# Kernel optimization log

Hardware: AMD Instinct MI355X
Metric: run time of the kernel (lower is better)

Reference implementation:

```python
import jax, jax.numpy as jnp
import numpy as np

N = 100000      # nodes
E = 1600000     # edges (avg degree 16)
D_IN, D_H, D_OUT = 128, 128, 64
NORM_SCALE = 1.0
EPS = 1e-6


def setup_inputs() -> dict:
    key = jax.random.key(0)
    ks = jax.random.split(key, 9)
    x = jax.random.normal(ks[0], (N, D_IN), dtype=jnp.float32)
    edge_index = jax.random.randint(ks[1], (2, E), 0, N, dtype=jnp.int32)
    edge_weight = jax.random.uniform(ks[2], (E,), dtype=jnp.float32)
    # GraphConv = Linear then spmm(adj, .); Glorot-ish init for weights
    W0 = jax.random.normal(ks[3], (D_IN, D_H), dtype=jnp.float32) / np.float32(np.sqrt(D_IN))
    b0 = jnp.zeros((D_H,), jnp.float32)
    W1 = jax.random.normal(ks[4], (D_H, D_H), dtype=jnp.float32) / np.float32(np.sqrt(D_H))
    b1 = jnp.zeros((D_H,), jnp.float32)
    Wout = jax.random.normal(ks[5], (D_H, D_OUT), dtype=jnp.float32) / np.float32(np.sqrt(D_H))
    bout = jnp.zeros((D_OUT,), jnp.float32)
    return {"x": x, "edge_index": edge_index, "edge_weight": edge_weight,
            "W0": W0, "b0": b0, "W1": W1, "b1": b1, "Wout": Wout, "bout": bout}


def _pair_norm(h):
    # PairNorm mode 'PN': center columns, divide by sqrt(mean squared row norm)
    h = h - jnp.mean(h, axis=0, keepdims=True)
    rownorm_mean = jnp.sqrt(EPS + jnp.mean(jnp.sum(h * h, axis=1)))
    return NORM_SCALE * h / rownorm_mean


def reference(x, edge_index, edge_weight, W0, b0, W1, b1, Wout, bout):
    src = edge_index[0]
    dst = edge_index[1]

    def graph_conv(h, W, b):
        h = h @ W + b                              # [N, d_out]
        msg = edge_weight[:, None] * h[src]        # [E, d_out] gather
        return jax.ops.segment_sum(msg, dst, num_segments=N)  # spmm(adj, h)

    x_old = jnp.zeros((), jnp.float32)
    for (W, b) in ((W0, b0), (W1, b1)):
        # dropout p=0 -> identity (omitted)
        h = graph_conv(x, W, b)
        h = jax.nn.relu(_pair_norm(h))
        x = h + x_old        # residual=1 -> skip every layer
        x_old = x
    return graph_conv(x, Wout, bout)
```

## Files before the change

### kernel.cpp

```cpp
#include <hip/hip_runtime.h>

#define N_NODES 100000
#define N_EDGES 1600000
#define DH 128
#define DOUT 64
#define EPS 1e-6f
#define NBINS 8
#define BINW 12500
#define NREP 64

__device__ inline unsigned bfround(float f) {
    unsigned u = __float_as_uint(f);
    return (u + 0x7fffu + ((u >> 16) & 1u)) >> 16;
}
__device__ inline unsigned pack2(float a, float b) { return bfround(a) | (bfround(b) << 16); }
__device__ inline float blo(unsigned u) { return __uint_as_float(u << 16); }
__device__ inline float bhi(unsigned u) { return __uint_as_float(u & 0xffff0000u); }

template <int COLS, int PN, bool OUTBF>
__global__ __launch_bounds__(256) void gemm_kernel(const float* __restrict__ Xa,
                                                   const float* __restrict__ muA,
                                                   const float* __restrict__ invA,
                                                   const float* __restrict__ Xb,
                                                   const float* __restrict__ muB,
                                                   const float* __restrict__ invB,
                                                   const float* __restrict__ W,
                                                   const float* __restrict__ bias,
                                                   void* __restrict__ Yv, int nrows) {
    constexpr int K = 128;
    constexpr int BK = 64;
    constexpr int COLG = COLS / 8;
    constexpr int ROWG = 256 / COLG;
    constexpr int RPT = 64 / ROWG;

    __shared__ float wlds[BK * COLS];
    __shared__ float xlds[64][BK + 1];

    const int tid = threadIdx.x;
    const int row0 = blockIdx.x * 64;

    const float sA = (PN >= 1) ? invA[0] : 0.f;
    const float sB = (PN == 2) ? invB[0] : 0.f;

    const int colg = tid % COLG;
    const int rowg = tid / COLG;
    const int c0 = colg * 8;
    const int r0 = rowg * RPT;

    float acc[RPT][8];
#pragma unroll
    for (int i = 0; i < RPT; ++i)
#pragma unroll
        for (int j = 0; j < 8; ++j) acc[i][j] = 0.f;

    for (int kb = 0; kb < K; kb += BK) {
        constexpr int WVEC = BK * COLS / 4;
        for (int i = tid; i < WVEC; i += 256) {
            int kr = i / (COLS / 4);
            int c4 = i % (COLS / 4);
            reinterpret_cast<float4*>(wlds)[i] =
                reinterpret_cast<const float4*>(W)[(size_t)(kb + kr) * (COLS / 4) + c4];
        }
        for (int i = tid; i < 64 * (BK / 4); i += 256) {
            int r = i / (BK / 4);
            int c4 = i % (BK / 4);
            int col4 = kb / 4 + c4;
            float4 v = make_float4(0.f, 0.f, 0.f, 0.f);
            if (row0 + r < nrows) {
                v = reinterpret_cast<const float4*>(Xa + (size_t)(row0 + r) * K)[col4];
                if constexpr (PN >= 1) {
                    float4 m = reinterpret_cast<const float4*>(muA)[col4];
                    v.x = fmaxf((v.x - m.x) * sA, 0.f);
                    v.y = fmaxf((v.y - m.y) * sA, 0.f);
                    v.z = fmaxf((v.z - m.z) * sA, 0.f);
                    v.w = fmaxf((v.w - m.w) * sA, 0.f);
                }
                if constexpr (PN == 2) {
                    float4 v2 = reinterpret_cast<const float4*>(Xb + (size_t)(row0 + r) * K)[col4];
                    float4 m2 = reinterpret_cast<const float4*>(muB)[col4];
                    v.x += fmaxf((v2.x - m2.x) * sB, 0.f);
                    v.y += fmaxf((v2.y - m2.y) * sB, 0.f);
                    v.z += fmaxf((v2.z - m2.z) * sB, 0.f);
                    v.w += fmaxf((v2.w - m2.w) * sB, 0.f);
                }
            }
            xlds[r][c4 * 4 + 0] = v.x;
            xlds[r][c4 * 4 + 1] = v.y;
            xlds[r][c4 * 4 + 2] = v.z;
            xlds[r][c4 * 4 + 3] = v.w;
        }
        __syncthreads();

        for (int k = 0; k < BK; ++k) {
            float4 w0 = *reinterpret_cast<const float4*>(&wlds[k * COLS + c0]);
            float4 w1 = *reinterpret_cast<const float4*>(&wlds[k * COLS + c0 + 4]);
#pragma unroll
            for (int i = 0; i < RPT; ++i) {
                float xv = xlds[r0 + i][k];
                acc[i][0] += xv * w0.x;
                acc[i][1] += xv * w0.y;
                acc[i][2] += xv * w0.z;
                acc[i][3] += xv * w0.w;
                acc[i][4] += xv * w1.x;
                acc[i][5] += xv * w1.y;
                acc[i][6] += xv * w1.z;
                acc[i][7] += xv * w1.w;
            }
        }
        __syncthreads();
    }

    float bv[8];
#pragma unroll
    for (int j = 0; j < 8; ++j) bv[j] = bias[c0 + j];

#pragma unroll
    for (int i = 0; i < RPT; ++i) {
        int row = row0 + r0 + i;
        if (row < nrows) {
#pragma unroll
            for (int j = 0; j < 8; ++j) acc[i][j] += bv[j];
            if constexpr (OUTBF) {
                uint4 q;
                q.x = pack2(acc[i][0], acc[i][1]);
                q.y = pack2(acc[i][2], acc[i][3]);
                q.z = pack2(acc[i][4], acc[i][5]);
                q.w = pack2(acc[i][6], acc[i][7]);
                *reinterpret_cast<uint4*>((unsigned*)Yv + (size_t)row * (COLS / 2) + (c0 >> 1)) = q;
            } else {
                float4 o0 = make_float4(acc[i][0], acc[i][1], acc[i][2], acc[i][3]);
                float4 o1 = make_float4(acc[i][4], acc[i][5], acc[i][6], acc[i][7]);
                float4* yp = reinterpret_cast<float4*>((float*)Yv + (size_t)row * COLS + c0);
                yp[0] = o0;
                yp[1] = o1;
            }
        }
    }
}

__global__ __launch_bounds__(256) void hist_kernel(const int* __restrict__ dst,
                                                   int* __restrict__ counts) {
    int e = blockIdx.x * blockDim.x + threadIdx.x;
    const int stride = gridDim.x * blockDim.x;
    for (; e < N_EDGES; e += stride) atomicAdd(&counts[dst[e]], 1);
}

__global__ __launch_bounds__(1024) void scan_kernel(const int* __restrict__ counts,
                                                    int* __restrict__ rowptr) {
    __shared__ int wsum[16];
    const int tid = threadIdx.x;
    const int lane = tid & 63;
    const int w = tid >> 6;
    int offset = 0;
    if (tid == 0) rowptr[0] = 0;
    for (int base = 0; base < N_NODES; base += 4096) {
        int i = base + tid * 4;
        int4 v = make_int4(0, 0, 0, 0);
        if (i < N_NODES) v = *reinterpret_cast<const int4*>(counts + i);
        int p0 = v.x, p1 = p0 + v.y, p2 = p1 + v.z, p3 = p2 + v.w;
        int incl = p3;
#pragma unroll
        for (int d = 1; d < 64; d <<= 1) {
            int t = __shfl_up(incl, d, 64);
            if (lane >= d) incl += t;
        }
        if (lane == 63) wsum[w] = incl;
        __syncthreads();
        if (w == 0 && lane < 16) {
            int t = wsum[lane];
#pragma unroll
            for (int d = 1; d < 16; d <<= 1) {
                int u = __shfl_up(t, d, 64);
                if (lane >= d) t += u;
            }
            wsum[lane] = t;
        }
        __syncthreads();
        int woff = (w == 0) ? 0 : wsum[w - 1];
        int chunk_total = wsum[15];
        int tbase = offset + woff + incl - p3;
        if (i < N_NODES) {
            rowptr[i + 1] = tbase + p0;
            rowptr[i + 2] = tbase + p1;
            rowptr[i + 3] = tbase + p2;
            rowptr[i + 4] = tbase + p3;
        }
        offset += chunk_total;
        __syncthreads();
    }
}

__global__ __launch_bounds__(256) void bucket_kernel(const int* __restrict__ src,
                                                     const int* __restrict__ dst,
                                                     const float* __restrict__ ew,
                                                     const int* __restrict__ rowptr,
                                                     int* __restrict__ fill,
                                                     int2* __restrict__ em) {
    const int myBin = blockIdx.x & (NBINS - 1);
    const int lo = myBin * BINW;
    const int hi = lo + BINW;
    int e = (blockIdx.x >> 3) * 256 + threadIdx.x;
    const int stride = (gridDim.x >> 3) * 256;
    for (; e < N_EDGES; e += stride) {
        int d = dst[e];
        if (d >= lo && d < hi) {
            int pos = atomicAdd(&fill[d], 1);
            em[rowptr[d] + pos] = make_int2(src[e], __float_as_int(ew[e]));
        }
    }
}

__global__ __launch_bounds__(256) void agg128b_kernel(const unsigned* __restrict__ Hb,
                                                      const int* __restrict__ rowptr,
                                                      const int2* __restrict__ em,
                                                      float* __restrict__ B,
                                                      float* __restrict__ cs_part,
                                                      float* __restrict__ ss_part) {
    __shared__ int2 smeta[4][64];
    __shared__ float cs[4][128];
    __shared__ float ssw[4];
    const int wv = threadIdx.x >> 6;
    const int lane = threadIdx.x & 63;
    const int node = blockIdx.x * 4 + wv;
    const int beg = rowptr[node];
    const int end = rowptr[node + 1];
    const int2* sm = smeta[wv];
    float ax0 = 0.f, ay0 = 0.f, ax1 = 0.f, ay1 = 0.f;

    for (int c = beg; c < end; c += 64) {
        smeta[wv][lane] = (c + lane < end) ? em[c + lane] : make_int2(0, 0);
        const int cnt = min(64, end - c);
        const int rounds = (cnt + 7) >> 3;
        for (int g = 0; g < rounds; ++g) {
            int2 m0 = sm[g * 8 + 0];
            int2 m1 = sm[g * 8 + 1];
            int2 m2 = sm[g * 8 + 2];
            int2 m3 = sm[g * 8 + 3];
            int2 m4 = sm[g * 8 + 4];
            int2 m5 = sm[g * 8 + 5];
            int2 m6 = sm[g * 8 + 6];
            int2 m7 = sm[g * 8 + 7];
            unsigned u0 = Hb[(size_t)m0.x * 64 + lane];
            unsigned u1 = Hb[(size_t)m1.x * 64 + lane];
            unsigned u2 = Hb[(size_t)m2.x * 64 + lane];
            unsigned u3 = Hb[(size_t)m3.x * 64 + lane];
            unsigned u4 = Hb[(size_t)m4.x * 64 + lane];
            unsigned u5 = Hb[(size_t)m5.x * 64 + lane];
            unsigned u6 = Hb[(size_t)m6.x * 64 + lane];
            unsigned u7 = Hb[(size_t)m7.x * 64 + lane];
            float w0 = __int_as_float(m0.y), w1 = __int_as_float(m1.y);
            float w2 = __int_as_float(m2.y), w3 = __int_as_float(m3.y);
            float w4 = __int_as_float(m4.y), w5 = __int_as_float(m5.y);
            float w6 = __int_as_float(m6.y), w7 = __int_as_float(m7.y);
            ax0 += w0 * blo(u0); ay0 += w0 * bhi(u0);
            ax1 += w1 * blo(u1); ay1 += w1 * bhi(u1);
            ax0 += w2 * blo(u2); ay0 += w2 * bhi(u2);
            ax1 += w3 * blo(u3); ay1 += w3 * bhi(u3);
            ax0 += w4 * blo(u4); ay0 += w4 * bhi(u4);
            ax1 += w5 * blo(u5); ay1 += w5 * bhi(u5);
            ax0 += w6 * blo(u6); ay0 += w6 * bhi(u6);
            ax1 += w7 * blo(u7); ay1 += w7 * bhi(u7);
        }
    }
    float2 acc = make_float2(ax0 + ax1, ay0 + ay1);
    reinterpret_cast<float2*>(B + (size_t)node * DH)[lane] = acc;

    cs[wv][lane * 2] = acc.x;
    cs[wv][lane * 2 + 1] = acc.y;
    float sq = acc.x * acc.x + acc.y * acc.y;
#pragma unroll
    for (int off = 32; off; off >>= 1) sq += __shfl_down(sq, off, 64);
    if (lane == 0) ssw[wv] = sq;
    __syncthreads();
    const int rep = blockIdx.x & (NREP - 1);
    if (threadIdx.x < 128) {
        float s = cs[0][threadIdx.x] + cs[1][threadIdx.x] + cs[2][threadIdx.x] + cs[3][threadIdx.x];
        atomicAdd(&cs_part[rep * 128 + threadIdx.x], s);
    }
    if (threadIdx.x == 0) atomicAdd(&ss_part[rep], ssw[0] + ssw[1] + ssw[2] + ssw[3]);
}

__global__ __launch_bounds__(256) void agg64b_kernel(const unsigned* __restrict__ Hb,
                                                     const int* __restrict__ rowptr,
                                                     const int2* __restrict__ em,
                                                     float* __restrict__ out) {
    __shared__ int2 smeta[4][64];
    const int wv = threadIdx.x >> 6;
    const int lane = threadIdx.x & 63;
    const int half = lane >> 5;
    const int col = lane & 31;
    const int node = blockIdx.x * 4 + wv;
    const int beg = rowptr[node];
    const int end = rowptr[node + 1];
    const int2* sm = smeta[wv];
    float ax0 = 0.f, ay0 = 0.f, ax1 = 0.f, ay1 = 0.f;

    for (int c = beg; c < end; c += 64) {
        smeta[wv][lane] = (c + lane < end) ? em[c + lane] : make_int2(0, 0);
        const int cnt = min(64, end - c);
        const int rounds = (cnt + 15) >> 4;
        for (int g = 0; g < rounds; ++g) {
            const int b = g * 16 + half;
            int2 m0 = sm[b + 0];
            int2 m1 = sm[b + 2];
            int2 m2 = sm[b + 4];
            int2 m3 = sm[b + 6];
            int2 m4 = sm[b + 8];
            int2 m5 = sm[b + 10];
            int2 m6 = sm[b + 12];
            int2 m7 = sm[b + 14];
            unsigned u0 = Hb[(size_t)m0.x * 32 + col];
            unsigned u1 = Hb[(size_t)m1.x * 32 + col];
            unsigned u2 = Hb[(size_t)m2.x * 32 + col];
            unsigned u3 = Hb[(size_t)m3.x * 32 + col];
            unsigned u4 = Hb[(size_t)m4.x * 32 + col];
            unsigned u5 = Hb[(size_t)m5.x * 32 + col];
            unsigned u6 = Hb[(size_t)m6.x * 32 + col];
            unsigned u7 = Hb[(size_t)m7.x * 32 + col];
            float w0 = __int_as_float(m0.y), w1 = __int_as_float(m1.y);
            float w2 = __int_as_float(m2.y), w3 = __int_as_float(m3.y);
            float w4 = __int_as_float(m4.y), w5 = __int_as_float(m5.y);
            float w6 = __int_as_float(m6.y), w7 = __int_as_float(m7.y);
            ax0 += w0 * blo(u0); ay0 += w0 * bhi(u0);
            ax1 += w1 * blo(u1); ay1 += w1 * bhi(u1);
            ax0 += w2 * blo(u2); ay0 += w2 * bhi(u2);
            ax1 += w3 * blo(u3); ay1 += w3 * bhi(u3);
            ax0 += w4 * blo(u4); ay0 += w4 * bhi(u4);
            ax1 += w5 * blo(u5); ay1 += w5 * bhi(u5);
            ax0 += w6 * blo(u6); ay0 += w6 * bhi(u6);
            ax1 += w7 * blo(u7); ay1 += w7 * bhi(u7);
        }
    }
    float ax = ax0 + ax1, ay = ay0 + ay1;
    ax += __shfl_xor(ax, 32, 64);
    ay += __shfl_xor(ay, 32, 64);
    if (lane < 32) {
        reinterpret_cast<float2*>(out + (size_t)node * DOUT)[col] = make_float2(ax, ay);
    }
}

__global__ void finalize_stats(const float* __restrict__ cs_part,
                               const float* __restrict__ ss_part, float* __restrict__ mu,
                               float* __restrict__ inv) {
    const int t = threadIdx.x;
    float m = 0.f;
    for (int r = 0; r < NREP; ++r) m += cs_part[r * 128 + t];
    float mean = m / (float)N_NODES;
    mu[t] = mean;
    float v = mean * mean;
    __shared__ float partl[2];
    __shared__ float sstot;
#pragma unroll
    for (int off = 32; off; off >>= 1) v += __shfl_down(v, off, 64);
    if ((t & 63) == 0) partl[t >> 6] = v;
    float ss = (t < NREP) ? ss_part[t] : 0.f;
#pragma unroll
    for (int off = 32; off; off >>= 1) ss += __shfl_down(ss, off, 64);
    if (t == 0) sstot = ss;
    __syncthreads();
    if (t == 0) {
        float musq = partl[0] + partl[1];
        float s = (sstot - (float)N_NODES * musq) / (float)N_NODES;
        inv[0] = rsqrtf(EPS + s);
    }
}

extern "C" void kernel_launch(void* const* d_in, const int* in_sizes, int n_in,
                              void* d_out, int out_size, void* d_ws, size_t ws_size,
                              hipStream_t stream) {
    const float* x = (const float*)d_in[0];
    const int* edge_index = (const int*)d_in[1];
    const float* ew = (const float*)d_in[2];
    const float* W0 = (const float*)d_in[3];
    const float* b0 = (const float*)d_in[4];
    const float* W1 = (const float*)d_in[5];
    const float* b1 = (const float*)d_in[6];
    const float* Wout = (const float*)d_in[7];
    const float* bout = (const float*)d_in[8];

    const int* src = edge_index;
    const int* dst = edge_index + N_EDGES;
    float* out = (float*)d_out;

    float* base = (float*)d_ws;
    unsigned* Hb = (unsigned*)base;
    float* B1 = base + (size_t)N_NODES * 64;
    float* B2 = B1 + (size_t)N_NODES * DH;
    int2* em = (int2*)(B2 + (size_t)N_NODES * DH);
    int* counts = (int*)(em + N_EDGES);
    int* fill = counts + N_NODES;
    int* rowptr = fill + N_NODES;
    size_t soff = (size_t)(rowptr + N_NODES + 1 - (int*)base);
    soff = (soff + 3) & ~(size_t)3;
    float* stats = base + soff;
    float* cs_part1 = stats;
    float* ss_part1 = cs_part1 + NREP * 128;
    float* cs_part2 = ss_part1 + NREP;
    float* ss_part2 = cs_part2 + NREP * 128;
    float* mu1 = ss_part2 + NREP;
    float* inv1 = mu1 + 128;
    float* mu2 = inv1 + 4;
    float* inv2 = mu2 + 128;

    const int gemm_grid = (N_NODES + 63) / 64;
    const int agg_grid = N_NODES / 4;

    hipMemsetAsync(counts, 0, (size_t)2 * N_NODES * sizeof(int), stream);
    hipMemsetAsync(stats, 0, (size_t)2 * (NREP * 128 + NREP) * sizeof(float), stream);

    hist_kernel<<<2048, 256, 0, stream>>>(dst, counts);
    scan_kernel<<<1, 1024, 0, stream>>>(counts, rowptr);
    bucket_kernel<<<2048, 256, 0, stream>>>(src, dst, ew, rowptr, fill, em);

    gemm_kernel<128, 0, true><<<gemm_grid, 256, 0, stream>>>(
        x, nullptr, nullptr, nullptr, nullptr, nullptr, W0, b0, Hb, N_NODES);
    agg128b_kernel<<<agg_grid, 256, 0, stream>>>(Hb, rowptr, em, B1, cs_part1, ss_part1);
    finalize_stats<<<1, 128, 0, stream>>>(cs_part1, ss_part1, mu1, inv1);

    gemm_kernel<128, 1, true><<<gemm_grid, 256, 0, stream>>>(
        B1, mu1, inv1, nullptr, nullptr, nullptr, W1, b1, Hb, N_NODES);
    agg128b_kernel<<<agg_grid, 256, 0, stream>>>(Hb, rowptr, em, B2, cs_part2, ss_part2);
    finalize_stats<<<1, 128, 0, stream>>>(cs_part2, ss_part2, mu2, inv2);

    gemm_kernel<64, 2, true><<<gemm_grid, 256, 0, stream>>>(
        B2, mu2, inv2, B1, mu1, inv1, Wout, bout, Hb, N_NODES);
    agg64b_kernel<<<agg_grid, 256, 0, stream>>>(Hb, rowptr, em, out);
}
```

Before: 589.9 us.

## Replace scalar FP32 GEMMs with bf16 MFMA kernels and vectorize histogram loads

The three dense GEMMs now run on MFMA 16x16x32 bf16 matrix instructions instead of scalar FP32 FMAs. Weights are converted to bf16 and stored transposed in swizzled LDS, and input rows are packed to bf16 with a swizzle to avoid bank conflicts. Each block now covers 128 rows in two 64-row passes. The degree histogram also loads destination indices as int4 and launches half the blocks. The bf16 GEMM inputs lower accuracy compared with the FP32 products, although the outputs were already rounded to bf16.

```diff
diff --git a/kernel.cpp b/kernel.cpp
--- a/kernel.cpp
+++ b/kernel.cpp
@@ -9,6 +9,9 @@
 #define BINW 12500
 #define NREP 64
 
+typedef __attribute__((ext_vector_type(8))) short s8v;
+typedef __attribute__((ext_vector_type(4))) float f32x4;
+
 __device__ inline unsigned bfround(float f) {
     unsigned u = __float_as_uint(f);
     return (u + 0x7fffu + ((u >> 16) & 1u)) >> 16;
@@ -17,122 +20,110 @@
 __device__ inline float blo(unsigned u) { return __uint_as_float(u << 16); }
 __device__ inline float bhi(unsigned u) { return __uint_as_float(u & 0xffff0000u); }
 
-template <int COLS, int PN, bool OUTBF>
-__global__ __launch_bounds__(256) void gemm_kernel(const float* __restrict__ Xa,
-                                                   const float* __restrict__ muA,
-                                                   const float* __restrict__ invA,
-                                                   const float* __restrict__ Xb,
-                                                   const float* __restrict__ muB,
-                                                   const float* __restrict__ invB,
-                                                   const float* __restrict__ W,
-                                                   const float* __restrict__ bias,
-                                                   void* __restrict__ Yv, int nrows) {
-    constexpr int K = 128;
-    constexpr int BK = 64;
-    constexpr int COLG = COLS / 8;
-    constexpr int ROWG = 256 / COLG;
-    constexpr int RPT = 64 / ROWG;
-
-    __shared__ float wlds[BK * COLS];
-    __shared__ float xlds[64][BK + 1];
+template <int COLS, int PN>
+__global__ __launch_bounds__(256) void gemm_mfma(const float* __restrict__ Xa,
+                                                 const float* __restrict__ muA,
+                                                 const float* __restrict__ invA,
+                                                 const float* __restrict__ Xb,
+                                                 const float* __restrict__ muB,
+                                                 const float* __restrict__ invB,
+                                                 const float* __restrict__ W,
+                                                 const float* __restrict__ bias,
+                                                 unsigned* __restrict__ Y, int nrows) {
+    constexpr int CT = COLS / 16;
+    __shared__ unsigned wtu[COLS][64];
+    __shared__ unsigned xbu[64][64];
 
     const int tid = threadIdx.x;
-    const int row0 = blockIdx.x * 64;
-
+    const int wv = tid >> 6;
+    const int lane = tid & 63;
     const float sA = (PN >= 1) ? invA[0] : 0.f;
     const float sB = (PN == 2) ? invB[0] : 0.f;
 
-    const int colg = tid % COLG;
-    const int rowg = tid / COLG;
-    const int c0 = colg * 8;
-    const int r0 = rowg * RPT;
-
-    float acc[RPT][8];
-#pragma unroll
-    for (int i = 0; i < RPT; ++i)
-#pragma unroll
-        for (int j = 0; j < 8; ++j) acc[i][j] = 0.f;
-
-    for (int kb = 0; kb < K; kb += BK) {
-        constexpr int WVEC = BK * COLS / 4;
-        for (int i = tid; i < WVEC; i += 256) {
-            int kr = i / (COLS / 4);
+    {
+        ushort* wts = (ushort*)wtu;
+        constexpr int NV4 = 128 * COLS / 4;
+        for (int i = tid; i < NV4; i += 256) {
+            int k = i / (COLS / 4);
             int c4 = i % (COLS / 4);
-            reinterpret_cast<float4*>(wlds)[i] =
-                reinterpret_cast<const float4*>(W)[(size_t)(kb + kr) * (COLS / 4) + c4];
-        }
-        for (int i = tid; i < 64 * (BK / 4); i += 256) {
-            int r = i / (BK / 4);
-            int c4 = i % (BK / 4);
-            int col4 = kb / 4 + c4;
+            float4 w4 = reinterpret_cast<const float4*>(W)[i];
+            float vals[4] = {w4.x, w4.y, w4.z, w4.w};
+            int u = k >> 1, kb = k & 1;
+#pragma unroll
+            for (int j = 0; j < 4; ++j) {
+                int c = c4 * 4 + j;
+                int us = u ^ ((c & 7) << 2);
+                wts[c * 128 + us * 2 + kb] = (ushort)bfround(vals[j]);
+            }
+        }
+    }
+
+    float bv[CT];
+#pragma unroll
+    for (int f = 0; f < CT; ++f) bv[f] = bias[f * 16 + (lane & 15)];
+
+    const int row0 = blockIdx.x * 128;
+    const int myr = (wv << 4) + (lane & 15);
+
+#pragma unroll
+    for (int ms = 0; ms < 2; ++ms) {
+        const int rb = row0 + ms * 64;
+        __syncthreads();
+        for (int i = tid; i < 2048; i += 256) {
+            int r = i >> 5;
+            int c4 = i & 31;
             float4 v = make_float4(0.f, 0.f, 0.f, 0.f);
-            if (row0 + r < nrows) {
-                v = reinterpret_cast<const float4*>(Xa + (size_t)(row0 + r) * K)[col4];
+            if (rb + r < nrows) {
+                v = reinterpret_cast<const float4*>(Xa + (size_t)(rb + r) * 128)[c4];
                 if constexpr (PN >= 1) {
-                    float4 m = reinterpret_cast<const float4*>(muA)[col4];
+                    float4 m = reinterpret_cast<const float4*>(muA)[c4];
                     v.x = fmaxf((v.x - m.x) * sA, 0.f);
                     v.y = fmaxf((v.y - m.y) * sA, 0.f);
                     v.z = fmaxf((v.z - m.z) * sA, 0.f);
                     v.w = fmaxf((v.w - m.w) * sA, 0.f);
                 }
                 if constexpr (PN == 2) {
-                    float4 v2 = reinterpret_cast<const float4*>(Xb + (size_t)(row0 + r) * K)[col4];
-                    float4 m2 = reinterpret_cast<const float4*>(muB)[col4];
+                    float4 v2 = reinterpret_cast<const float4*>(Xb + (size_t)(rb + r) * 128)[c4];
+                    float4 m2 = reinterpret_cast<const float4*>(muB)[c4];
                     v.x += fmaxf((v2.x - m2.x) * sB, 0.f);
                     v.y += fmaxf((v2.y - m2.y) * sB, 0.f);
                     v.z += fmaxf((v2.z - m2.z) * sB, 0.f);
                     v.w += fmaxf((v2.w - m2.w) * sB, 0.f);
                 }
             }
-            xlds[r][c4 * 4 + 0] = v.x;
-            xlds[r][c4 * 4 + 1] = v.y;
-            xlds[r][c4 * 4 + 2] = v.z;
-            xlds[r][c4 * 4 + 3] = v.w;
+            int sw = (r & 7) << 2;
+            xbu[r][(c4 * 2) ^ sw] = pack2(v.x, v.y);
+            xbu[r][(c4 * 2 + 1) ^ sw] = pack2(v.z, v.w);
         }
         __syncthreads();
 
-        for (int k = 0; k < BK; ++k) {
-            float4 w0 = *reinterpret_cast<const float4*>(&wlds[k * COLS + c0]);
-            float4 w1 = *reinterpret_cast<const float4*>(&wlds[k * COLS + c0 + 4]);
-#pragma unroll
-            for (int i = 0; i < RPT; ++i) {
-                float xv = xlds[r0 + i][k];
-                acc[i][0] += xv * w0.x;
-                acc[i][1] += xv * w0.y;
-                acc[i][2] += xv * w0.z;
-                acc[i][3] += xv * w0.w;
-                acc[i][4] += xv * w1.x;
-                acc[i][5] += xv * w1.y;
-                acc[i][6] += xv * w1.z;
-                acc[i][7] += xv * w1.w;
+        f32x4 acc[CT];
+#pragma unroll
+        for (int f = 0; f < CT; ++f) acc[f] = (f32x4){0.f, 0.f, 0.f, 0.f};
+        const int xsw = (myr & 7) << 2;
+#pragma unroll
+        for (int kc = 0; kc < 4; ++kc) {
+            const int u0 = kc * 16 + (lane >> 4) * 4;
+            s8v a = *reinterpret_cast<const s8v*>(&xbu[myr][u0 ^ xsw]);
+#pragma unroll
+            for (int f = 0; f < CT; ++f) {
+                const int c = f * 16 + (lane & 15);
+                s8v b = *reinterpret_cast<const s8v*>(&wtu[c][u0 ^ ((c & 7) << 2)]);
+                acc[f] = __builtin_amdgcn_mfma_f32_16x16x32_bf16(a, b, acc[f], 0, 0, 0);
             }
         }
-        __syncthreads();
-    }
-
-    float bv[8];
-#pragma unroll
-    for (int j = 0; j < 8; ++j) bv[j] = bias[c0 + j];
-
-#pragma unroll
-    for (int i = 0; i < RPT; ++i) {
-        int row = row0 + r0 + i;
-        if (row < nrows) {
-#pragma unroll
-            for (int j = 0; j < 8; ++j) acc[i][j] += bv[j];
-            if constexpr (OUTBF) {
-                uint4 q;
-                q.x = pack2(acc[i][0], acc[i][1]);
-                q.y = pack2(acc[i][2], acc[i][3]);
-                q.z = pack2(acc[i][4], acc[i][5]);
-                q.w = pack2(acc[i][6], acc[i][7]);
-                *reinterpret_cast<uint4*>((unsigned*)Yv + (size_t)row * (COLS / 2) + (c0 >> 1)) = q;
-            } else {
-                float4 o0 = make_float4(acc[i][0], acc[i][1], acc[i][2], acc[i][3]);
-                float4 o1 = make_float4(acc[i][4], acc[i][5], acc[i][6], acc[i][7]);
-                float4* yp = reinterpret_cast<float4*>((float*)Yv + (size_t)row * COLS + c0);
-                yp[0] = o0;
-                yp[1] = o1;
+
+#pragma unroll
+        for (int f = 0; f < CT; ++f) {
+#pragma unroll
+            for (int r = 0; r < 4; ++r) {
+                float v = acc[f][r] + bv[f];
+                float p = __shfl_xor(v, 1, 64);
+                unsigned pk = (lane & 1) ? pack2(p, v) : pack2(v, p);
+                int grow = rb + (wv << 4) + ((lane >> 4) << 2) + r;
+                if (grow < nrows && ((lane & 1) == (f & 1))) {
+                    Y[(size_t)grow * (COLS / 2) + f * 8 + ((lane & 15) >> 1)] = pk;
+                }
             }
         }
     }
@@ -140,9 +131,15 @@
 
 __global__ __launch_bounds__(256) void hist_kernel(const int* __restrict__ dst,
                                                    int* __restrict__ counts) {
-    int e = blockIdx.x * blockDim.x + threadIdx.x;
+    int i = blockIdx.x * blockDim.x + threadIdx.x;
     const int stride = gridDim.x * blockDim.x;
-    for (; e < N_EDGES; e += stride) atomicAdd(&counts[dst[e]], 1);
+    for (; i < N_EDGES / 4; i += stride) {
+        int4 d = reinterpret_cast<const int4*>(dst)[i];
+        atomicAdd(&counts[d.x], 1);
+        atomicAdd(&counts[d.y], 1);
+        atomicAdd(&counts[d.z], 1);
+        atomicAdd(&counts[d.w], 1);
+    }
 }
 
 __global__ __launch_bounds__(1024) void scan_kernel(const int* __restrict__ counts,
@@ -402,27 +399,27 @@
     float* mu2 = inv1 + 4;
     float* inv2 = mu2 + 128;
 
-    const int gemm_grid = (N_NODES + 63) / 64;
+    const int gemm_grid = (N_NODES + 127) / 128;
     const int agg_grid = N_NODES / 4;
 
     hipMemsetAsync(counts, 0, (size_t)2 * N_NODES * sizeof(int), stream);
     hipMemsetAsync(stats, 0, (size_t)2 * (NREP * 128 + NREP) * sizeof(float), stream);
 
-    hist_kernel<<<2048, 256, 0, stream>>>(dst, counts);
+    hist_kernel<<<1024, 256, 0, stream>>>(dst, counts);
     scan_kernel<<<1, 1024, 0, stream>>>(counts, rowptr);
     bucket_kernel<<<2048, 256, 0, stream>>>(src, dst, ew, rowptr, fill, em);
 
-    gemm_kernel<128, 0, true><<<gemm_grid, 256, 0, stream>>>(
+    gemm_mfma<128, 0><<<gemm_grid, 256, 0, stream>>>(
         x, nullptr, nullptr, nullptr, nullptr, nullptr, W0, b0, Hb, N_NODES);
     agg128b_kernel<<<agg_grid, 256, 0, stream>>>(Hb, rowptr, em, B1, cs_part1, ss_part1);
     finalize_stats<<<1, 128, 0, stream>>>(cs_part1, ss_part1, mu1, inv1);
 
-    gemm_kernel<128, 1, true><<<gemm_grid, 256, 0, stream>>>(
+    gemm_mfma<128, 1><<<gemm_grid, 256, 0, stream>>>(
         B1, mu1, inv1, nullptr, nullptr, nullptr, W1, b1, Hb, N_NODES);
     agg128b_kernel<<<agg_grid, 256, 0, stream>>>(Hb, rowptr, em, B2, cs_part2, ss_part2);
     finalize_stats<<<1, 128, 0, stream>>>(cs_part2, ss_part2, mu2, inv2);
 
-    gemm_kernel<64, 2, true><<<gemm_grid, 256, 0, stream>>>(
+    gemm_mfma<64, 2><<<gemm_grid, 256, 0, stream>>>(
         B2, mu2, inv2, B1, mu1, inv1, Wout, bout, Hb, N_NODES);
     agg64b_kernel<<<agg_grid, 256, 0, stream>>>(Hb, rowptr, em, out);
 }
```

New measurement: 556.7 us. 1.06x faster.
